# Kernel optimization log

Measured on AMD Instinct MI355X. Metric: run time of the kernel, lower is better.

Reference implementation:

```python
import jax, jax.numpy as jnp
import numpy as np

NEG_SLOPE = 0.2
EPS = 1e-16


def _add_self_loops(edge_index, edge_weight, N):
    # PyG add_self_loops with fill_value='mean': self-loop attr = mean of
    # incoming edge attrs per node (0 if node has no incoming edges).
    src, dst = edge_index[0], edge_index[1]
    ones = jnp.ones_like(edge_weight)
    cnt = jax.ops.segment_sum(ones, dst, num_segments=N)
    wsum = jax.ops.segment_sum(edge_weight, dst, num_segments=N)
    self_w = jnp.where(cnt > 0, wsum / jnp.maximum(cnt, 1.0), 0.0)
    loop = jnp.arange(N, dtype=src.dtype)
    return (jnp.concatenate([src, loop]), jnp.concatenate([dst, loop]),
            jnp.concatenate([edge_weight, self_w]))


def _gatv2_layer(x, src, dst, ew, Wl, Wr, att, We, bias, N):
    # x: [M, N, Din]; src/dst: [E']; ew: [E']; att: [H, C]
    M = x.shape[0]
    H, C = att.shape
    xl = (x @ Wl).reshape(M, N, H, C)   # source transform (lin_l)
    xr = (x @ Wr).reshape(M, N, H, C)   # target transform (lin_r)
    xj = xl[:, src]                      # [M, E', H, C] gather source feats
    xi = xr[:, dst]                      # [M, E', H, C] gather target feats
    ee = (ew[:, None] @ We).reshape(-1, H, C)  # [E', H, C] edge embedding
    s = jax.nn.leaky_relu(xi + xj + ee[None], NEG_SLOPE)
    logits = jnp.einsum('mehc,hc->meh', s, att)  # [M, E', H]
    # segment softmax over edges grouped by destination node
    smax = jax.vmap(lambda u: jax.ops.segment_max(u, dst, num_segments=N))(logits)
    a = jnp.exp(logits - smax[:, dst])
    denom = jax.vmap(lambda u: jax.ops.segment_sum(u, dst, num_segments=N))(a)
    alpha = a / (denom[:, dst] + EPS)
    msg = alpha[..., None] * xj          # [M, E', H, C]
    out = jax.vmap(lambda u: jax.ops.segment_sum(u, dst, num_segments=N))(msg)
    return out.reshape(M, N, H * C) + bias


def setup_inputs() -> dict:
    key = jax.random.key(0)
    ks = jax.random.split(key, 14)
    B, T, N, Din = 2, 8, 5000, 64
    E, H, OUT = 80000, 2, 128
    C = OUT // H  # 64
    g = jax.nn.initializers.glorot_uniform()
    inp = {
        'x': jax.random.normal(ks[0], (B, T, N, Din), jnp.float32),
        'edge_index': jax.random.randint(ks[1], (2, E), 0, N, jnp.int32),
        'edge_weight': jax.random.uniform(ks[2], (E,), jnp.float32),
        # conv1 params
        'Wl1': g(ks[3], (Din, H * C), jnp.float32),
        'Wr1': g(ks[4], (Din, H * C), jnp.float32),
        'att1': g(ks[5], (H, C), jnp.float32),
        'We1': g(ks[6], (1, H * C), jnp.float32),
        'b1': jnp.zeros((H * C,), jnp.float32),
        # conv2 params
        'Wl2': g(ks[7], (OUT, H * C), jnp.float32),
        'Wr2': g(ks[8], (OUT, H * C), jnp.float32),
        'att2': g(ks[9], (H, C), jnp.float32),
        'We2': g(ks[10], (1, H * C), jnp.float32),
        'b2': jnp.zeros((H * C,), jnp.float32),
    }
    return inp


def reference(x, edge_index, edge_weight, Wl1, Wr1, att1, We1, b1,
              Wl2, Wr2, att2, We2, b2):
    B, T, N, Din = x.shape
    M = B * T
    # Tiling edges by B*T with node offsets is equivalent to sharing the same
    # edge list across M independent graph copies -> vectorize over M.
    src, dst, ew = _add_self_loops(edge_index, edge_weight, N)
    h = x.reshape(M, N, Din)
    h = _gatv2_layer(h, src, dst, ew, Wl1, Wr1, att1, We1, b1, N)
    h = jax.nn.elu(h)
    h = _gatv2_layer(h, src, dst, ew, Wl2, Wr2, att2, We2, b2, N)
    h = jax.nn.elu(h)
    return h.reshape(B, T, N, -1)
```

## Files before the change

kernel.cpp:

```cpp
#include <hip/hip_runtime.h>
#include <cstdint>
#include <cstddef>

static constexpr float NEG_SLOPE_C = 0.2f;
static constexpr float EPS_C = 1e-16f;
static constexpr float LOG2E_C = 1.4426950408889634f;

#if defined(__has_builtin)
#if __has_builtin(__builtin_amdgcn_exp2f)
#define EXP2F(x) __builtin_amdgcn_exp2f(x)
#else
#define EXP2F(x) exp2f(x)
#endif
#else
#define EXP2F(x) exp2f(x)
#endif

typedef __attribute__((ext_vector_type(8))) short bf16x8;
typedef __attribute__((ext_vector_type(4))) float f32x4;
typedef __attribute__((ext_vector_type(2))) float f32x2;

__device__ __forceinline__ f32x2 pk_add(f32x2 a, f32x2 b) {
    f32x2 d;
    asm("v_pk_add_f32 %0, %1, %2" : "=v"(d) : "v"(a), "v"(b));
    return d;
}
__device__ __forceinline__ f32x2 pk_mul(f32x2 a, f32x2 b) {
    f32x2 d;
    asm("v_pk_mul_f32 %0, %1, %2" : "=v"(d) : "v"(a), "v"(b));
    return d;
}
__device__ __forceinline__ f32x2 pk_fma(f32x2 a, f32x2 b, f32x2 c) {
    f32x2 d;
    asm("v_pk_fma_f32 %0, %1, %2, %3" : "=v"(d) : "v"(a), "v"(b), "v"(c));
    return d;
}
__device__ __forceinline__ f32x2 pk_abs(f32x2 a) {
    f32x2 d;
    d.x = __builtin_fabsf(a.x);
    d.y = __builtin_fabsf(a.y);
    return d;
}

__device__ __forceinline__ short bf16_rne(float x) {
    unsigned u = __float_as_uint(x);
    u = (u + 0x7FFF + ((u >> 16) & 1)) >> 16;
    return (short)u;
}
__device__ __forceinline__ float bf16f(short s) {
    return __uint_as_float(((unsigned)(unsigned short)s) << 16);
}

template<int CTRL>
__device__ __forceinline__ float dpp_add_f(float v) {
    int x = __builtin_amdgcn_update_dpp(0, __float_as_int(v), CTRL, 0xf, 0xf, true);
    return v + __int_as_float(x);
}

__device__ __forceinline__ float reduce16(float q) {
    q = dpp_add_f<0xB1>(q);
    q = dpp_add_f<0x4E>(q);
    q = dpp_add_f<0x141>(q);
    q = dpp_add_f<0x140>(q);
    return q;
}


__device__ __forceinline__ void wprep_body(const float* __restrict__ Wl,
                                           const float* __restrict__ Wr,
                                           uint4* __restrict__ Wf, int gid) {
    const int lane = gid & 63;
    const int t = (gid >> 6) & 15;
    const int s = gid >> 10;
    const int mr = lane & 15, q = lane >> 4;
    const int col = t * 16 + mr;
    const float* src = (col < 128) ? (Wl + col) : (Wr + col - 128);
    union { short sh[8]; uint4 u; } hv, lv;
    #pragma unroll
    for (int j = 0; j < 8; ++j) {
        const float v = src[(size_t)(s * 32 + q * 8 + j) * 128];
        const short h = bf16_rne(v);
        hv.sh[j] = h;
        lv.sh[j] = bf16_rne(v - bf16f(h));
    }
    const size_t base = (size_t)s * 2048 + (size_t)(t * 2) * 64 + lane;
    Wf[base] = hv.u;
    Wf[base + 64] = lv.u;
}

__global__ void prep_kernel(const int* __restrict__ ei, const float* __restrict__ ew,
                            int E, int eb,
                            int* __restrict__ cursor, float* __restrict__ wsum,
                            int2* __restrict__ pairs,
                            const float* __restrict__ Wl1, const float* __restrict__ Wr1,
                            uint4* __restrict__ wf1,
                            const float* __restrict__ Wl2, const float* __restrict__ Wr2,
                            uint4* __restrict__ wf2) {
    const int blk = blockIdx.x;
    if (blk < eb) {
        const int e = blk * 256 + threadIdx.x;
        if (e >= E) return;
        const int dst = ei[E + e];
        const float w = ew[e];
        const int idx = atomicAdd(&cursor[dst], 1);
        atomicAdd(&wsum[dst], w);
        if (idx < 64)
            pairs[(size_t)dst * 64 + idx] = make_int2(ei[e] * 512, __float_as_int(w));
    } else if (blk < eb + 8) {
        wprep_body(Wl1, Wr1, wf1, (blk - eb) * 256 + threadIdx.x);
    } else {
        wprep_body(Wl2, Wr2, wf2, (blk - eb - 8) * 256 + threadIdx.x);
    }
}


template<int K>
__global__ __launch_bounds__(256) void gemm_mfma_kernel(
    const float* __restrict__ X, const uint4* __restrict__ Wf,
    float* __restrict__ outL, float* __restrict__ outR) {
    __shared__ uint4 xbuf[8 * 64];
    const int tid = threadIdx.x;
    const int w = tid >> 6;
    const int lane = tid & 63;
    const int q = lane >> 4;
    const int mr = lane & 15;
    const int blockRow = blockIdx.x * 64;

    const int srow = lane;
    const float* sxp = X + (size_t)(blockRow + srow) * K + w * 8;
    const int sdst = ((srow >> 4) * 2) * 64 + w * 16 + (srow & 15);

    f32x4 acc[4][4];
    #pragma unroll
    for (int tt = 0; tt < 4; ++tt)
        #pragma unroll
        for (int r = 0; r < 4; ++r)
            acc[tt][r] = (f32x4){0.f, 0.f, 0.f, 0.f};

    for (int s = 0; s < K / 32; ++s) {
        const float4 a0 = *(const float4*)(sxp + s * 32);
        const float4 a1 = *(const float4*)(sxp + s * 32 + 4);
        union { short sh[8]; uint4 u; } hv, lv;
        {
            const float av[8] = {a0.x, a0.y, a0.z, a0.w, a1.x, a1.y, a1.z, a1.w};
            #pragma unroll
            for (int jj = 0; jj < 8; ++jj) {
                const short h = bf16_rne(av[jj]);
                hv.sh[jj] = h;
                lv.sh[jj] = bf16_rne(av[jj] - bf16f(h));
            }
        }
        __syncthreads();
        xbuf[sdst] = hv.u;
        xbuf[sdst + 64] = lv.u;
        __syncthreads();

        bf16x8 xh[4], xl[4];
        #pragma unroll
        for (int r = 0; r < 4; ++r) {
            xh[r] = *(const bf16x8*)&xbuf[(r * 2) * 64 + lane];
            xl[r] = *(const bf16x8*)&xbuf[(r * 2 + 1) * 64 + lane];
        }
        const uint4* wp = Wf + (size_t)s * 2048 + (size_t)(4 * w) * 128 + lane;
        #pragma unroll
        for (int tt = 0; tt < 4; ++tt) {
            const bf16x8 wh = *(const bf16x8*)&wp[tt * 128];
            const bf16x8 wl = *(const bf16x8*)&wp[tt * 128 + 64];
            #pragma unroll
            for (int r = 0; r < 4; ++r) {
                acc[tt][r] = __builtin_amdgcn_mfma_f32_16x16x32_bf16(wh, xh[r], acc[tt][r], 0, 0, 0);
                acc[tt][r] = __builtin_amdgcn_mfma_f32_16x16x32_bf16(wl, xh[r], acc[tt][r], 0, 0, 0);
                acc[tt][r] = __builtin_amdgcn_mfma_f32_16x16x32_bf16(wh, xl[r], acc[tt][r], 0, 0, 0);
            }
        }
    }

    float* const obase = (w < 2) ? outL : outR;
    const int cbase = (w & 1) * 64 + q * 4;
    #pragma unroll
    for (int tt = 0; tt < 4; ++tt) {
        #pragma unroll
        for (int r = 0; r < 4; ++r) {
            const size_t o = (size_t)(blockRow + r * 16 + mr) * 128 + cbase + tt * 16;
            *(float4*)(obase + o) =
                make_float4(acc[tt][r][0], acc[tt][r][1], acc[tt][r][2], acc[tt][r][3]);
        }
    }
}


__global__ __launch_bounds__(256) void edge_kernel(
    const float* __restrict__ xl, const float* __restrict__ xr,
    const int* __restrict__ degp, const float* __restrict__ wsum,
    const int2* __restrict__ pairs,
    const float* __restrict__ att, const float* __restrict__ We,
    const float* __restrict__ bias, float* __restrict__ out,
    int N, int M) {
    const int wave = __builtin_amdgcn_readfirstlane(threadIdx.x >> 6);
    const int b = blockIdx.x;
    const int hb = (b >= 10000) ? (b - 10000) : b;
    const int m = ((b >= 10000) ? 8 : 0) + (hb & 7);
    const int n = (hb >> 3) * 4 + wave;
    if (n >= N) return;
    const int lane = threadIdx.x & 63;
    const int j = lane & 31;
    const bool hi = lane >= 32;
    const int h4 = (lane >> 5) << 2;
    const int j16 = j << 4;

    const char* xlp = (const char*)(xl + (size_t)m * N * 128);
    const char* xrp = (const char*)(xr + (size_t)m * N * 128);

    const int2 myp = pairs[((size_t)n << 6) + lane];
    const int deg = min(degp[n], 64);

    f32x2 a06_01, a06_23, a04_01, a04_23, we01, we23, xi01, xi23;
    {
        const float4 at4 = ((const float4*)att)[j];
        const float4 we4 = ((const float4*)We)[j];
        const float4 xi4 = *(const float4*)(xrp + (size_t)n * 512 + j16);
        const float c06 = 0.6f * LOG2E_C, c04 = 0.4f * LOG2E_C;
        a06_01 = (f32x2){at4.x * c06, at4.y * c06};
        a06_23 = (f32x2){at4.z * c06, at4.w * c06};
        a04_01 = (f32x2){at4.x * c04, at4.y * c04};
        a04_23 = (f32x2){at4.z * c04, at4.w * c04};
        we01 = (f32x2){we4.x, we4.y};
        we23 = (f32x2){we4.z, we4.w};
        xi01 = (f32x2){xi4.x, xi4.y};
        xi23 = (f32x2){xi4.z, xi4.w};
    }

    float base, lsum;
    f32x2 acc01, acc23;
    {
        const float sw = (deg > 0) ? (wsum[n] / (float)deg) : 0.0f;
        const f32x2 sw2 = (f32x2){sw, sw};
        const float4 xj4 = *(const float4*)(xlp + (size_t)n * 512 + j16);
        const f32x2 s01 = pk_fma(sw2, we01, pk_add(xi01, (f32x2){xj4.x, xj4.y}));
        const f32x2 s23 = pk_fma(sw2, we23, pk_add(xi23, (f32x2){xj4.z, xj4.w}));
        f32x2 q01 = pk_mul(a06_01, s01);
        q01 = pk_fma(a04_01, pk_abs(s01), q01);
        f32x2 q23 = pk_mul(a06_23, s23);
        q23 = pk_fma(a04_23, pk_abs(s23), q23);
        const f32x2 qp = pk_add(q01, q23);
        base = reduce16(qp.x + qp.y);
        lsum = 0.5f;
        acc01 = (f32x2){xj4.x * 0.5f, xj4.y * 0.5f};
        acc23 = (f32x2){xj4.z * 0.5f, xj4.w * 0.5f};
    }

    auto BODY = [&](f32x2 w2, float4 xj4, bool mask) {
        const f32x2 xj01 = (f32x2){xj4.x, xj4.y};
        const f32x2 xj23 = (f32x2){xj4.z, xj4.w};
        const f32x2 s01 = pk_fma(w2, we01, pk_add(xi01, xj01));
        const f32x2 s23 = pk_fma(w2, we23, pk_add(xi23, xj23));
        f32x2 q01 = pk_mul(a06_01, s01);
        q01 = pk_fma(a04_01, pk_abs(s01), q01);
        f32x2 q23 = pk_mul(a06_23, s23);
        q23 = pk_fma(a04_23, pk_abs(s23), q23);
        const f32x2 qp = pk_add(q01, q23);
        const float q = reduce16(qp.x + qp.y);
        float t = EXP2F(q - base);
        if (mask) t = hi ? 0.f : t;
        lsum += t;
        const f32x2 t2 = (f32x2){t, t};
        acc01 = pk_fma(t2, xj01, acc01);
        acc23 = pk_fma(t2, xj23, acc23);
    };

    if (deg > 0) {
        const int niter = (deg + 1) >> 1;
        const bool odd = (deg & 1) != 0;

        auto PULL = [&](int s, int& ro, f32x2& w2) {
            const int idx = (s << 3) + h4;
            ro = __builtin_amdgcn_ds_bpermute(idx, myp.x);
            const int wb = __builtin_amdgcn_ds_bpermute(idx, myp.y);
            w2.x = __int_as_float(wb);
            w2.y = w2.x;
        };
        auto GATH = [&](int ro) -> float4 {
            return *(const float4*)(xlp + (unsigned)(ro + j16));
        };

        int roA, roB, roC, roD;
        f32x2 wA, wB, wC, wD;
        PULL(0, roA, wA);
        PULL(1, roB, wB);
        PULL(2, roC, wC);
        PULL(3, roD, wD);
        float4 xA = GATH(roA);
        float4 xB = GATH(roB);
        float4 xC, xD;

        int k = 0;
        while (k + 4 < niter) {
            xC = GATH(roC);
            xD = GATH(roD);
            __builtin_amdgcn_sched_barrier(0);
            BODY(wA, xA, false);
            PULL(k + 4, roA, wA);
            BODY(wB, xB, false);
            PULL(k + 5, roB, wB);
            xA = GATH(roA);
            xB = GATH(roB);
            __builtin_amdgcn_sched_barrier(0);
            BODY(wC, xC, false);
            PULL(k + 6, roC, wC);
            BODY(wD, xD, false);
            PULL(k + 7, roD, wD);
            k += 4;
        }
        const int rem = niter - k;
        if (rem >= 3) xC = GATH(roC);
        if (rem == 4) xD = GATH(roD);
        BODY(wA, xA, odd && (rem == 1));
        if (rem >= 2) BODY(wB, xB, odd && (rem == 2));
        if (rem >= 3) BODY(wC, xC, odd && (rem == 3));
        if (rem == 4) BODY(wD, xD, odd);
    }

    lsum += __shfl_xor(lsum, 32, 64);
    acc01.x += __shfl_xor(acc01.x, 32, 64);
    acc01.y += __shfl_xor(acc01.y, 32, 64);
    acc23.x += __shfl_xor(acc23.x, 32, 64);
    acc23.y += __shfl_xor(acc23.y, 32, 64);

    const float inv = 1.f / (lsum + EPS_C);
    const float4 b4 = ((const float4*)bias)[j];
    float o0 = fmaf(acc01.x, inv, b4.x);
    float o1 = fmaf(acc01.y, inv, b4.y);
    float o2 = fmaf(acc23.x, inv, b4.z);
    float o3 = fmaf(acc23.y, inv, b4.w);
    o0 = o0 > 0.f ? o0 : (__expf(o0) - 1.f);
    o1 = o1 > 0.f ? o1 : (__expf(o1) - 1.f);
    o2 = o2 > 0.f ? o2 : (__expf(o2) - 1.f);
    o3 = o3 > 0.f ? o3 : (__expf(o3) - 1.f);
    if (!hi) {
        ((float4*)(out + (size_t)m * N * 128))[n * 32 + j] =
            make_float4(o0, o1, o2, o3);
    }
}


extern "C" void kernel_launch(void* const* d_in, const int* in_sizes, int n_in,
                              void* d_out, int out_size, void* d_ws, size_t ws_size,
                              hipStream_t stream) {
    const float* x    = (const float*)d_in[0];
    const int*   ei   = (const int*)d_in[1];
    const float* ew   = (const float*)d_in[2];
    const float* Wl1  = (const float*)d_in[3];
    const float* Wr1  = (const float*)d_in[4];
    const float* att1 = (const float*)d_in[5];
    const float* We1  = (const float*)d_in[6];
    const float* b1   = (const float*)d_in[7];
    const float* Wl2  = (const float*)d_in[8];
    const float* Wr2  = (const float*)d_in[9];
    const float* att2 = (const float*)d_in[10];
    const float* We2  = (const float*)d_in[11];
    const float* b2   = (const float*)d_in[12];

    const int E = in_sizes[1] / 2;
    const int N = 5000;
    const int R = out_size / 128;
    const int M = R / N;

    char* ws = (char*)d_ws;
    size_t off = 0;
    auto alloc = [&](size_t bytes) {
        char* p = ws + off;
        off = (off + bytes + 255) & ~(size_t)255;
        return p;
    };
    int*   cursor = (int*)  alloc((size_t)N * 4);
    float* wsum   = (float*)alloc((size_t)N * 4);
    int2*  pairs  = (int2*) alloc((size_t)N * 64 * 8);
    uint4* wf1    = (uint4*)alloc((size_t)2 * 2048 * 16);
    uint4* wf2    = (uint4*)alloc((size_t)4 * 2048 * 16);
    float* bufA   = (float*)alloc((size_t)R * 128 * 4);
    float* bufB   = (float*)alloc((size_t)R * 128 * 4);
    float* bufC   = (float*)alloc((size_t)R * 128 * 4);

    const size_t zspan = (size_t)((char*)(pairs + (size_t)N * 64) - (char*)cursor);
    hipMemsetAsync(cursor, 0, zspan, stream);

    const int eb = (E + 255) / 256;
    prep_kernel<<<eb + 24, 256, 0, stream>>>(ei, ew, E, eb, cursor, wsum, pairs,
                                             Wl1, Wr1, wf1, Wl2, Wr2, wf2);

    const int gb = R / 64;
    const int tb = 2 * ((N + 3) / 4) * 8;

    gemm_mfma_kernel<64><<<gb, 256, 0, stream>>>(x, wf1, bufA, bufB);
    edge_kernel<<<tb, 256, 0, stream>>>(bufA, bufB, cursor, wsum, pairs,
                                        att1, We1, b1, bufC, N, M);
    gemm_mfma_kernel<128><<<gb, 256, 0, stream>>>(bufC, wf2, bufA, bufB);
    edge_kernel<<<tb, 256, 0, stream>>>(bufA, bufB, cursor, wsum, pairs,
                                        att2, We2, b2, (float*)d_out, N, M);
}
```

Baseline: 264.1 us.

## Process four destination nodes per wave and prefetch their per-node data upfront

Each wave in the edge kernel now handles four consecutive destination nodes instead of one, and the grid shrinks fourfold. Before the per-node loops start, it batch-loads each node's pair list, degree, weight sum, and target and self features, so those loads overlap. The aim is to cut per-wave setup overhead and hide load latency across nodes. The cost is fewer waves in flight, higher register pressure, and serialised per-node work inside a wave, which may reduce latency hiding for the gathers. The vector loads of degp and wsum at nb can read past N, though only at the last group where N is a multiple of 4.

```diff
diff --git a/kernel.cpp b/kernel.cpp
--- a/kernel.cpp
+++ b/kernel.cpp
@@ -198,10 +198,11 @@
     int N, int M) {
     const int wave = __builtin_amdgcn_readfirstlane(threadIdx.x >> 6);
     const int b = blockIdx.x;
-    const int hb = (b >= 10000) ? (b - 10000) : b;
-    const int m = ((b >= 10000) ? 8 : 0) + (hb & 7);
-    const int n = (hb >> 3) * 4 + wave;
-    if (n >= N) return;
+    const bool half = b >= 2504;
+    const int hb = half ? b - 2504 : b;
+    const int m = (half ? 8 : 0) + (hb & 7);
+    const int nb = (hb >> 3) * 16 + wave * 4;
+    if (nb >= N) return;
     const int lane = threadIdx.x & 63;
     const int j = lane & 31;
     const bool hi = lane >= 32;
@@ -211,14 +212,28 @@
     const char* xlp = (const char*)(xl + (size_t)m * N * 128);
     const char* xrp = (const char*)(xr + (size_t)m * N * 128);
 
-    const int2 myp = pairs[((size_t)n << 6) + lane];
-    const int deg = min(degp[n], 64);
-
-    f32x2 a06_01, a06_23, a04_01, a04_23, we01, we23, xi01, xi23;
+    const int n1 = min(nb + 1, N - 1);
+    const int n2 = min(nb + 2, N - 1);
+    const int n3 = min(nb + 3, N - 1);
+    const int2 myp0 = pairs[((size_t)nb << 6) + lane];
+    const int2 myp1 = pairs[((size_t)n1 << 6) + lane];
+    const int2 myp2 = pairs[((size_t)n2 << 6) + lane];
+    const int2 myp3 = pairs[((size_t)n3 << 6) + lane];
+    const int4  dg = *(const int4*)&degp[nb];
+    const float4 wsm = *(const float4*)&wsum[nb];
+    const float4 xi_0 = *(const float4*)(xrp + (size_t)nb * 512 + j16);
+    const float4 xi_1 = *(const float4*)(xrp + (size_t)n1 * 512 + j16);
+    const float4 xi_2 = *(const float4*)(xrp + (size_t)n2 * 512 + j16);
+    const float4 xi_3 = *(const float4*)(xrp + (size_t)n3 * 512 + j16);
+    const float4 xs_0 = *(const float4*)(xlp + (size_t)nb * 512 + j16);
+    const float4 xs_1 = *(const float4*)(xlp + (size_t)n1 * 512 + j16);
+    const float4 xs_2 = *(const float4*)(xlp + (size_t)n2 * 512 + j16);
+    const float4 xs_3 = *(const float4*)(xlp + (size_t)n3 * 512 + j16);
+
+    f32x2 a06_01, a06_23, a04_01, a04_23, we01, we23;
     {
         const float4 at4 = ((const float4*)att)[j];
         const float4 we4 = ((const float4*)We)[j];
-        const float4 xi4 = *(const float4*)(xrp + (size_t)n * 512 + j16);
         const float c06 = 0.6f * LOG2E_C, c04 = 0.4f * LOG2E_C;
         a06_01 = (f32x2){at4.x * c06, at4.y * c06};
         a06_23 = (f32x2){at4.z * c06, at4.w * c06};
@@ -226,120 +241,129 @@
         a04_23 = (f32x2){at4.z * c04, at4.w * c04};
         we01 = (f32x2){we4.x, we4.y};
         we23 = (f32x2){we4.z, we4.w};
-        xi01 = (f32x2){xi4.x, xi4.y};
-        xi23 = (f32x2){xi4.z, xi4.w};
     }
-
-    float base, lsum;
-    f32x2 acc01, acc23;
-    {
-        const float sw = (deg > 0) ? (wsum[n] / (float)deg) : 0.0f;
-        const f32x2 sw2 = (f32x2){sw, sw};
-        const float4 xj4 = *(const float4*)(xlp + (size_t)n * 512 + j16);
-        const f32x2 s01 = pk_fma(sw2, we01, pk_add(xi01, (f32x2){xj4.x, xj4.y}));
-        const f32x2 s23 = pk_fma(sw2, we23, pk_add(xi23, (f32x2){xj4.z, xj4.w}));
-        f32x2 q01 = pk_mul(a06_01, s01);
-        q01 = pk_fma(a04_01, pk_abs(s01), q01);
-        f32x2 q23 = pk_mul(a06_23, s23);
-        q23 = pk_fma(a04_23, pk_abs(s23), q23);
-        const f32x2 qp = pk_add(q01, q23);
-        base = reduce16(qp.x + qp.y);
-        lsum = 0.5f;
-        acc01 = (f32x2){xj4.x * 0.5f, xj4.y * 0.5f};
-        acc23 = (f32x2){xj4.z * 0.5f, xj4.w * 0.5f};
-    }
-
-    auto BODY = [&](f32x2 w2, float4 xj4, bool mask) {
-        const f32x2 xj01 = (f32x2){xj4.x, xj4.y};
-        const f32x2 xj23 = (f32x2){xj4.z, xj4.w};
-        const f32x2 s01 = pk_fma(w2, we01, pk_add(xi01, xj01));
-        const f32x2 s23 = pk_fma(w2, we23, pk_add(xi23, xj23));
-        f32x2 q01 = pk_mul(a06_01, s01);
-        q01 = pk_fma(a04_01, pk_abs(s01), q01);
-        f32x2 q23 = pk_mul(a06_23, s23);
-        q23 = pk_fma(a04_23, pk_abs(s23), q23);
-        const f32x2 qp = pk_add(q01, q23);
-        const float q = reduce16(qp.x + qp.y);
-        float t = EXP2F(q - base);
-        if (mask) t = hi ? 0.f : t;
-        lsum += t;
-        const f32x2 t2 = (f32x2){t, t};
-        acc01 = pk_fma(t2, xj01, acc01);
-        acc23 = pk_fma(t2, xj23, acc23);
+    const float4 b4 = ((const float4*)bias)[j];
+
+    auto PROCESS = [&](int n, int2 myp, int degr, float wsv,
+                       float4 xi4, float4 xjs) {
+        const f32x2 xi01 = (f32x2){xi4.x, xi4.y};
+        const f32x2 xi23 = (f32x2){xi4.z, xi4.w};
+        const int deg = min(degr, 64);
+
+        float base, lsum;
+        f32x2 acc01, acc23;
+        {
+            const float sw = (deg > 0) ? (wsv / (float)deg) : 0.0f;
+            const f32x2 sw2 = (f32x2){sw, sw};
+            const f32x2 s01 = pk_fma(sw2, we01, pk_add(xi01, (f32x2){xjs.x, xjs.y}));
+            const f32x2 s23 = pk_fma(sw2, we23, pk_add(xi23, (f32x2){xjs.z, xjs.w}));
+            f32x2 q01 = pk_mul(a06_01, s01);
+            q01 = pk_fma(a04_01, pk_abs(s01), q01);
+            f32x2 q23 = pk_mul(a06_23, s23);
+            q23 = pk_fma(a04_23, pk_abs(s23), q23);
+            const f32x2 qp = pk_add(q01, q23);
+            base = reduce16(qp.x + qp.y);
+            lsum = 0.5f;
+            acc01 = (f32x2){xjs.x * 0.5f, xjs.y * 0.5f};
+            acc23 = (f32x2){xjs.z * 0.5f, xjs.w * 0.5f};
+        }
+
+        auto BODY = [&](f32x2 w2, float4 xj4, bool mask) {
+            const f32x2 xj01 = (f32x2){xj4.x, xj4.y};
+            const f32x2 xj23 = (f32x2){xj4.z, xj4.w};
+            const f32x2 s01 = pk_fma(w2, we01, pk_add(xi01, xj01));
+            const f32x2 s23 = pk_fma(w2, we23, pk_add(xi23, xj23));
+            f32x2 q01 = pk_mul(a06_01, s01);
+            q01 = pk_fma(a04_01, pk_abs(s01), q01);
+            f32x2 q23 = pk_mul(a06_23, s23);
+            q23 = pk_fma(a04_23, pk_abs(s23), q23);
+            const f32x2 qp = pk_add(q01, q23);
+            const float q = reduce16(qp.x + qp.y);
+            float t = EXP2F(q - base);
+            if (mask) t = hi ? 0.f : t;
+            lsum += t;
+            const f32x2 t2 = (f32x2){t, t};
+            acc01 = pk_fma(t2, xj01, acc01);
+            acc23 = pk_fma(t2, xj23, acc23);
+        };
+
+        if (deg > 0) {
+            const int niter = (deg + 1) >> 1;
+            const bool odd = (deg & 1) != 0;
+
+            auto PULL = [&](int s, int& ro, f32x2& w2) {
+                const int idx = (s << 3) + h4;
+                ro = __builtin_amdgcn_ds_bpermute(idx, myp.x);
+                const int wb = __builtin_amdgcn_ds_bpermute(idx, myp.y);
+                w2.x = __int_as_float(wb);
+                w2.y = w2.x;
+            };
+            auto GATH = [&](int ro) -> float4 {
+                return *(const float4*)(xlp + (unsigned)(ro + j16));
+            };
+
+            int roA, roB, roC, roD;
+            f32x2 wA, wB, wC, wD;
+            PULL(0, roA, wA);
+            PULL(1, roB, wB);
+            PULL(2, roC, wC);
+            PULL(3, roD, wD);
+            float4 xA = GATH(roA);
+            float4 xB = GATH(roB);
+            float4 xC, xD;
+
+            int k = 0;
+            while (k + 4 < niter) {
+                xC = GATH(roC);
+                xD = GATH(roD);
+                __builtin_amdgcn_sched_barrier(0);
+                BODY(wA, xA, false);
+                PULL(k + 4, roA, wA);
+                BODY(wB, xB, false);
+                PULL(k + 5, roB, wB);
+                xA = GATH(roA);
+                xB = GATH(roB);
+                __builtin_amdgcn_sched_barrier(0);
+                BODY(wC, xC, false);
+                PULL(k + 6, roC, wC);
+                BODY(wD, xD, false);
+                PULL(k + 7, roD, wD);
+                k += 4;
+            }
+            const int rem = niter - k;
+            if (rem >= 3) xC = GATH(roC);
+            if (rem == 4) xD = GATH(roD);
+            BODY(wA, xA, odd && (rem == 1));
+            if (rem >= 2) BODY(wB, xB, odd && (rem == 2));
+            if (rem >= 3) BODY(wC, xC, odd && (rem == 3));
+            if (rem == 4) BODY(wD, xD, odd);
+        }
+
+        lsum += __shfl_xor(lsum, 32, 64);
+        acc01.x += __shfl_xor(acc01.x, 32, 64);
+        acc01.y += __shfl_xor(acc01.y, 32, 64);
+        acc23.x += __shfl_xor(acc23.x, 32, 64);
+        acc23.y += __shfl_xor(acc23.y, 32, 64);
+
+        const float inv = 1.f / (lsum + EPS_C);
+        float o0 = fmaf(acc01.x, inv, b4.x);
+        float o1 = fmaf(acc01.y, inv, b4.y);
+        float o2 = fmaf(acc23.x, inv, b4.z);
+        float o3 = fmaf(acc23.y, inv, b4.w);
+        o0 = o0 > 0.f ? o0 : (__expf(o0) - 1.f);
+        o1 = o1 > 0.f ? o1 : (__expf(o1) - 1.f);
+        o2 = o2 > 0.f ? o2 : (__expf(o2) - 1.f);
+        o3 = o3 > 0.f ? o3 : (__expf(o3) - 1.f);
+        if (!hi) {
+            ((float4*)(out + (size_t)m * N * 128))[n * 32 + j] =
+                make_float4(o0, o1, o2, o3);
+        }
     };
 
-    if (deg > 0) {
-        const int niter = (deg + 1) >> 1;
-        const bool odd = (deg & 1) != 0;
-
-        auto PULL = [&](int s, int& ro, f32x2& w2) {
-            const int idx = (s << 3) + h4;
-            ro = __builtin_amdgcn_ds_bpermute(idx, myp.x);
-            const int wb = __builtin_amdgcn_ds_bpermute(idx, myp.y);
-            w2.x = __int_as_float(wb);
-            w2.y = w2.x;
-        };
-        auto GATH = [&](int ro) -> float4 {
-            return *(const float4*)(xlp + (unsigned)(ro + j16));
-        };
-
-        int roA, roB, roC, roD;
-        f32x2 wA, wB, wC, wD;
-        PULL(0, roA, wA);
-        PULL(1, roB, wB);
-        PULL(2, roC, wC);
-        PULL(3, roD, wD);
-        float4 xA = GATH(roA);
-        float4 xB = GATH(roB);
-        float4 xC, xD;
-
-        int k = 0;
-        while (k + 4 < niter) {
-            xC = GATH(roC);
-            xD = GATH(roD);
-            __builtin_amdgcn_sched_barrier(0);
-            BODY(wA, xA, false);
-            PULL(k + 4, roA, wA);
-            BODY(wB, xB, false);
-            PULL(k + 5, roB, wB);
-            xA = GATH(roA);
-            xB = GATH(roB);
-            __builtin_amdgcn_sched_barrier(0);
-            BODY(wC, xC, false);
-            PULL(k + 6, roC, wC);
-            BODY(wD, xD, false);
-            PULL(k + 7, roD, wD);
-            k += 4;
-        }
-        const int rem = niter - k;
-        if (rem >= 3) xC = GATH(roC);
-        if (rem == 4) xD = GATH(roD);
-        BODY(wA, xA, odd && (rem == 1));
-        if (rem >= 2) BODY(wB, xB, odd && (rem == 2));
-        if (rem >= 3) BODY(wC, xC, odd && (rem == 3));
-        if (rem == 4) BODY(wD, xD, odd);
-    }
-
-    lsum += __shfl_xor(lsum, 32, 64);
-    acc01.x += __shfl_xor(acc01.x, 32, 64);
-    acc01.y += __shfl_xor(acc01.y, 32, 64);
-    acc23.x += __shfl_xor(acc23.x, 32, 64);
-    acc23.y += __shfl_xor(acc23.y, 32, 64);
-
-    const float inv = 1.f / (lsum + EPS_C);
-    const float4 b4 = ((const float4*)bias)[j];
-    float o0 = fmaf(acc01.x, inv, b4.x);
-    float o1 = fmaf(acc01.y, inv, b4.y);
-    float o2 = fmaf(acc23.x, inv, b4.z);
-    float o3 = fmaf(acc23.y, inv, b4.w);
-    o0 = o0 > 0.f ? o0 : (__expf(o0) - 1.f);
-    o1 = o1 > 0.f ? o1 : (__expf(o1) - 1.f);
-    o2 = o2 > 0.f ? o2 : (__expf(o2) - 1.f);
-    o3 = o3 > 0.f ? o3 : (__expf(o3) - 1.f);
-    if (!hi) {
-        ((float4*)(out + (size_t)m * N * 128))[n * 32 + j] =
-            make_float4(o0, o1, o2, o3);
-    }
+    PROCESS(nb, myp0, dg.x, wsm.x, xi_0, xs_0);
+    if (nb + 1 < N) PROCESS(nb + 1, myp1, dg.y, wsm.y, xi_1, xs_1);
+    if (nb + 2 < N) PROCESS(nb + 2, myp2, dg.z, wsm.z, xi_2, xs_2);
+    if (nb + 3 < N) PROCESS(nb + 3, myp3, dg.w, wsm.w, xi_3, xs_3);
 }
 
 
@@ -389,7 +413,7 @@
                                              Wl1, Wr1, wf1, Wl2, Wr2, wf2);
 
     const int gb = R / 64;
-    const int tb = 2 * ((N + 3) / 4) * 8;
+    const int tb = 2 * ((N + 15) / 16) * 8;
 
     gemm_mfma_kernel<64><<<gb, 256, 0, stream>>>(x, wf1, bufA, bufB);
     edge_kernel<<<tb, 256, 0, stream>>>(bufA, bufB, cursor, wsum, pairs,
```

After: 271.7 us. 1.03x slower.
